# Performance work log

Measured on AMD Instinct MI355X. Metric: run time of the kernel, lower is better.

Reference implementation:

```python
import jax, jax.numpy as jnp
import numpy as np

B, S, H = 64, 512, 768
ATT_H, CLS_H = 100, 300


def setup_inputs() -> dict:
    key = jax.random.key(0)
    ks = jax.random.split(key, 8)
    hidden_states = jax.random.normal(ks[0], (B, S, H), jnp.float32)
    is_cont = jax.random.bernoulli(ks[1], 0.25, (B, S)).at[:, 0].set(False)
    offset_mapping = jnp.stack(
        [is_cont.astype(jnp.int32) * 3, jnp.zeros((B, S), jnp.int32)], axis=-1
    )
    labels = jax.random.randint(ks[2], (B, S), -1, 2).astype(jnp.float32)
    s = 0.02
    W1 = jax.random.normal(ks[3], (H, ATT_H), jnp.float32) * s
    b1 = jnp.zeros((ATT_H,), jnp.float32)
    W2 = jax.random.normal(ks[4], (ATT_H, 1), jnp.float32) * s
    b2 = jnp.zeros((1,), jnp.float32)
    W3 = jax.random.normal(ks[5], (H, CLS_H), jnp.float32) * s
    b3 = jnp.zeros((CLS_H,), jnp.float32)
    W4 = jax.random.normal(ks[6], (CLS_H, 1), jnp.float32) * s
    b4 = jnp.zeros((1,), jnp.float32)
    return dict(hidden_states=hidden_states, offset_mapping=offset_mapping,
                labels=labels, W1=W1, b1=b1, W2=W2, b2=b2, W3=W3, b3=b3,
                W4=W4, b4=b4)


def reference(hidden_states, offset_mapping, labels, W1, b1, W2, b2, W3, b3, W4, b4):
    beta = 1.0            # soft_attention_beta
    w_sent, w_tok, w_reg = 1.0, 1.0, 0.01
    Bn, Sn, _ = hidden_states.shape

    # token attention head: sigmoid(tanh(h W1 + b1) W2 + b2) -> [B, S]
    token_att = jax.nn.sigmoid(jnp.tanh(hidden_states @ W1 + b1) @ W2 + b2)[..., 0]

    # --- subword grouping as a single segment-max ---
    # a continuation token (offset[...,0] != 0) belongs to the segment started
    # by the previous non-continuation token (the word root).
    is_cont = offset_mapping[:, :, 0] != 0          # [B, S]
    start = jnp.logical_not(is_cont)
    start_flat = start.reshape(-1)
    seg_id = jnp.cumsum(start_flat.astype(jnp.int32)) - 1   # [B*S]
    vals = token_att.reshape(-1)
    seg_red = jax.ops.segment_max(vals, seg_id, num_segments=Bn * Sn)  # 'max' subword_method
    # scatter the group reduction back onto the word-root position only
    word_att = jnp.where(start_flat, seg_red[seg_id], vals).reshape(Bn, Sn)

    # mask: labelled (!= -1) AND not a subword continuation
    mask = (jnp.logical_and(labels != -1.0, start)).astype(hidden_states.dtype)
    masked = word_att * mask                          # token_logits

    # soft attention pooling over sequence
    p = jnp.power(masked, beta)
    norm = p / jnp.sum(p, axis=1, keepdims=True)      # [B, S]
    pooled = jnp.einsum('bsh,bs->bh', hidden_states, norm)

    sent = jax.nn.sigmoid(jnp.tanh(pooled @ W3 + b3) @ W4 + b4)  # [B, 1]

    # --- losses (_calculate_loss) ---
    sent_labels = jnp.max(labels, axis=1, keepdims=True)          # [B, 1]
    sentence_loss = jnp.sum((sent - sent_labels) ** 2)
    zero_labels = jnp.where(labels == 1.0, labels, 0.0)
    token_loss = jnp.sum((masked - zero_labels) ** 2)
    ones_mask = jnp.where(masked == 0.0, 1.0, masked)
    reg_a = jnp.sum(jnp.min(ones_mask, axis=1, keepdims=True) ** 2)
    reg_b = jnp.sum((jnp.max(masked, axis=1, keepdims=True) - sent_labels) ** 2)
    loss = w_sent * sentence_loss + w_tok * token_loss + w_reg * (reg_a + reg_b)

    return (loss, sentence_loss, token_loss, reg_a, reg_b,
            hidden_states, masked, sent)
```

## Files before the change

kernel.cpp:

```cpp
#include <hip/hip_runtime.h>
#include <math.h>

#define Bn 64
#define Sn 512
#define Hn 768
#define ATT_H 100
#define CLS_H 300
#define Mtok (Bn*Sn)
#define NP 112
#define NT 7

#define W1T_N (NP*Hn)
#define W3T_N (CLS_H*Hn)
#define POOL_N (Bn*Hn)

#define KCH 256
#define LDA2 264

typedef __attribute__((ext_vector_type(8))) short short8;
typedef __attribute__((ext_vector_type(4))) float floatx4;

__device__ inline float sigf(float x) { return 1.0f / (1.0f + expf(-x)); }

__device__ inline unsigned short f2bf(float x) {
    union { float f; unsigned int u; } v; v.f = x;
    unsigned int r = (v.u + 0x7FFFu + ((v.u >> 16) & 1u)) >> 16;
    return (unsigned short)r;
}

__device__ inline float wred_sum(float v) {
    #pragma unroll
    for (int d = 32; d; d >>= 1) v += __shfl_down(v, d, 64);
    return v;
}
__device__ inline float wred_max(float v) {
    #pragma unroll
    for (int d = 32; d; d >>= 1) v = fmaxf(v, __shfl_down(v, d, 64));
    return v;
}
__device__ inline float wred_min(float v) {
    #pragma unroll
    for (int d = 32; d; d >>= 1) v = fminf(v, __shfl_down(v, d, 64));
    return v;
}

__global__ __launch_bounds__(256) void k0_prep(
    const float* __restrict__ W1, const float* __restrict__ b1,
    const float* __restrict__ W2, const float* __restrict__ W3,
    unsigned short* __restrict__ w1t, float* __restrict__ b1w2,
    float* __restrict__ w3t, float* __restrict__ pooled,
    float* __restrict__ zpart)
{
    int idx = blockIdx.x * 256 + threadIdx.x;
    if (idx < W1T_N) {
        int n = idx / Hn, k = idx - n * Hn;
        float v = (n < ATT_H) ? W1[(size_t)k * ATT_H + n] : 0.f;
        w1t[idx] = f2bf(v);
    } else if (idx < W1T_N + W3T_N) {
        int i = idx - W1T_N;
        int j = i / Hn, k = i - j * Hn;
        w3t[i] = W3[(size_t)k * CLS_H + j];
    } else if (idx < W1T_N + W3T_N + NP) {
        int j = idx - (W1T_N + W3T_N);
        b1w2[2 * j]     = (j < ATT_H) ? b1[j] : 0.f;
        b1w2[2 * j + 1] = (j < ATT_H) ? W2[j] : 0.f;
    } else if (idx < W1T_N + W3T_N + NP + POOL_N) {
        pooled[idx - (W1T_N + W3T_N + NP)] = 0.f;
    } else if (idx < W1T_N + W3T_N + NP + POOL_N + 5 * Bn) {
        zpart[idx - (W1T_N + W3T_N + NP + POOL_N)] = 0.f;
    }
}

__global__ __launch_bounds__(512, 4) void k1_att(
    const float* __restrict__ h, const unsigned short* __restrict__ w1t,
    const float* __restrict__ b1w2, const float* __restrict__ b2,
    float* __restrict__ out_hidden, float* __restrict__ att)
{
    __shared__ unsigned short As[64 * LDA2];

    const int tid = threadIdx.x;
    const int wave = tid >> 6, lane = tid & 63;
    const int u = lane & 15, q = lane >> 4;
    const int tl = wave & 3, g = wave >> 2;
    const int t0 = blockIdx.x * 64;
    const int srow = tid >> 6, sc4 = tid & 63;

    floatx4 acc[NT];
    #pragma unroll
    for (int ct = 0; ct < NT; ct++) acc[ct] = (floatx4)0.f;

    for (int it = 0; it < 3; it++) {
        __syncthreads();
        #pragma unroll
        for (int j = 0; j < 8; j++) {
            int row = srow + j * 8;
            size_t gidx = (size_t)(t0 + row) * Hn + it * KCH + sc4 * 4;
            floatx4 v = *(const floatx4*)(h + gidx);
            *(floatx4*)(out_hidden + gidx) = v;
            ushort4 bv;
            bv.x = f2bf(v.x); bv.y = f2bf(v.y);
            bv.z = f2bf(v.z); bv.w = f2bf(v.w);
            *(ushort4*)(&As[row * LDA2 + sc4 * 4]) = bv;
        }
        __syncthreads();
        #pragma unroll
        for (int kk = 0; kk < 4; kk++) {
            short8 a = *(const short8*)(&As[(tl * 16 + u) * LDA2 + g * 128 + kk * 32 + q * 8]);
            #pragma unroll
            for (int ct = 0; ct < NT; ct++) {
                const short8* bp = (const short8*)(w1t + (size_t)(ct * 16 + u) * Hn
                                                   + it * KCH + g * 128 + kk * 32 + q * 8);
                acc[ct] = __builtin_amdgcn_mfma_f32_16x16x32_bf16(a, *bp, acc[ct], 0, 0, 0);
            }
        }
    }

    __syncthreads();
    float* cb = (float*)As;
    if (g == 1) {
        #pragma unroll
        for (int ct = 0; ct < NT; ct++)
            *(floatx4*)(&cb[(tl * 64 + lane) * 28 + ct * 4]) = acc[ct];
    }
    __syncthreads();
    if (g == 0) {
        #pragma unroll
        for (int ct = 0; ct < NT; ct++) {
            floatx4 o = *(const floatx4*)(&cb[(tl * 64 + lane) * 28 + ct * 4]);
            acc[ct] += o;
        }
        float z[4] = {0.f, 0.f, 0.f, 0.f};
        #pragma unroll
        for (int ct = 0; ct < NT; ct++) {
            float2 bw = *(const float2*)(b1w2 + (ct * 16 + u) * 2);
            #pragma unroll
            for (int r = 0; r < 4; r++)
                z[r] += tanhf(acc[ct][r] + bw.x) * bw.y;
        }
        #pragma unroll
        for (int mask = 1; mask < 16; mask <<= 1) {
            #pragma unroll
            for (int r = 0; r < 4; r++) z[r] += __shfl_xor(z[r], mask, 64);
        }
        if (u == 0) {
            float bb2 = b2[0];
            #pragma unroll
            for (int r = 0; r < 4; r++)
                att[t0 + tl * 16 + q * 4 + r] = sigf(z[r] + bb2);
        }
    }
}

__global__ __launch_bounds__(256) void k2_seg(
    const float* __restrict__ att, const int* __restrict__ offset,
    const float* __restrict__ labels, float* __restrict__ masked_out,
    float* __restrict__ sum_m, float* __restrict__ slab_o,
    float* __restrict__ tl_o, float* __restrict__ mino_o,
    float* __restrict__ maxm_o)
{
    const int b = blockIdx.x, tid = threadIdx.x;
    __shared__ float attl[Sn];
    __shared__ int   startl[Sn];
    __shared__ float v0[Sn], v1[Sn];
    __shared__ int   f0[Sn], f1[Sn];
    __shared__ float rsum[4], rtl[4], rsl[4], rmn[4], rmx[4];

    for (int s = tid; s < Sn; s += 256) {
        attl[s] = att[b * Sn + s];
        startl[s] = (offset[(size_t)(b * Sn + s) * 2] == 0) ? 1 : 0;
    }
    __syncthreads();
    for (int i = tid; i < Sn; i += 256) {
        int s = Sn - 1 - i;
        int endf = (s == Sn - 1) ? 1 : startl[s + 1];
        v0[i] = attl[s];
        f0[i] = endf;
    }
    __syncthreads();

    float* va = v0; float* vb = v1;
    int* fa = f0; int* fb = f1;
    for (int d = 1; d < Sn; d <<= 1) {
        for (int i = tid; i < Sn; i += 256) {
            float v = va[i]; int f = fa[i];
            float nv = v; int nf = f;
            if (i >= d) {
                if (!f) nv = fmaxf(v, va[i - d]);
                nf = f | fa[i - d];
            }
            vb[i] = nv; fb[i] = nf;
        }
        __syncthreads();
        float* tv = va; va = vb; vb = tv;
        int* tf = fa; fa = fb; fb = tf;
    }

    float lsum = 0.f, ltl = 0.f, lslab = -1e30f, lmin = 1e30f, lmax = -1e30f;
    for (int s = tid; s < Sn; s += 256) {
        float lab = labels[b * Sn + s];
        int st = startl[s];
        float segm = va[Sn - 1 - s];
        float m = (st && lab != -1.0f) ? segm : 0.f;
        masked_out[b * Sn + s] = m;
        lsum += m;
        float zl = (lab == 1.0f) ? 1.f : 0.f;
        ltl += (m - zl) * (m - zl);
        lslab = fmaxf(lslab, lab);
        float om = (m == 0.f) ? 1.f : m;
        lmin = fminf(lmin, om);
        lmax = fmaxf(lmax, m);
    }
    int wid = tid >> 6, lane = tid & 63;
    lsum = wred_sum(lsum); ltl = wred_sum(ltl);
    lslab = wred_max(lslab); lmin = wred_min(lmin); lmax = wred_max(lmax);
    if (lane == 0) { rsum[wid]=lsum; rtl[wid]=ltl; rsl[wid]=lslab; rmn[wid]=lmin; rmx[wid]=lmax; }
    __syncthreads();
    if (tid == 0) {
        sum_m[b]  = rsum[0]+rsum[1]+rsum[2]+rsum[3];
        tl_o[b]   = rtl[0]+rtl[1]+rtl[2]+rtl[3];
        slab_o[b] = fmaxf(fmaxf(rsl[0],rsl[1]), fmaxf(rsl[2],rsl[3]));
        mino_o[b] = fminf(fminf(rmn[0],rmn[1]), fminf(rmn[2],rmn[3]));
        maxm_o[b] = fmaxf(fmaxf(rmx[0],rmx[1]), fmaxf(rmx[2],rmx[3]));
    }
}

__global__ __launch_bounds__(192) void k3_pool(
    const float* __restrict__ h, const float* __restrict__ masked,
    const float* __restrict__ sum_m, float* __restrict__ pooled)
{
    const int b = blockIdx.x, sc = blockIdx.y;
    const int tid = threadIdx.x;
    __shared__ float nrm[16];
    if (tid < 16)
        nrm[tid] = masked[b * Sn + sc * 16 + tid] * (1.0f / sum_m[b]);
    __syncthreads();
    const floatx4* hp = (const floatx4*)(h + ((size_t)b * Sn + sc * 16) * Hn) + tid;
    float ax = 0.f, ay = 0.f, az = 0.f, aw = 0.f;
    #pragma unroll 8
    for (int s = 0; s < 16; s++) {
        floatx4 v = hp[(size_t)s * (Hn / 4)];
        float w = nrm[s];
        ax += v.x * w; ay += v.y * w; az += v.z * w; aw += v.w * w;
    }
    float* pp = pooled + (size_t)b * Hn + tid * 4;
    atomicAdd(pp + 0, ax); atomicAdd(pp + 1, ay);
    atomicAdd(pp + 2, az); atomicAdd(pp + 3, aw);
}

__global__ __launch_bounds__(256) void k4_sent(
    const float* __restrict__ pooled, const float* __restrict__ w3t,
    const float* __restrict__ b3, const float* __restrict__ W4,
    float* __restrict__ zpart)
{
    const int b = blockIdx.x, jc = blockIdx.y;
    const int tid = threadIdx.x;
    __shared__ __align__(16) float pl[Hn];
    __shared__ float yred[64];
    for (int k = tid; k < Hn; k += 256) pl[k] = pooled[(size_t)b * Hn + k];
    if (tid < 64) yred[tid] = 0.f;
    __syncthreads();
    int jj = tid >> 2, ks = tid & 3;
    float a = 0.f;
    if (jj < 60) {
        int j = jc * 60 + jj;
        const floatx4* wr = (const floatx4*)(w3t + (size_t)j * Hn) + ks * 48;
        const floatx4* pr = (const floatx4*)pl + ks * 48;
        #pragma unroll 8
        for (int i = 0; i < 48; i++) {
            floatx4 wv = wr[i]; floatx4 pv = pr[i];
            a += wv.x * pv.x + wv.y * pv.y + wv.z * pv.z + wv.w * pv.w;
        }
    }
    a += __shfl_xor(a, 1, 64);
    a += __shfl_xor(a, 2, 64);
    if (jj < 60 && ks == 0) {
        int j = jc * 60 + jj;
        yred[jj] = tanhf(a + b3[j]) * W4[j];
    }
    __syncthreads();
    if (tid < 64) {
        float y = yred[tid];
        y = wred_sum(y);
        if (tid == 0) zpart[jc * Bn + b] = y;
    }
}

__global__ __launch_bounds__(64) void k5_loss(
    const float* __restrict__ zpart, const float* __restrict__ b4,
    const float* __restrict__ slab, const float* __restrict__ tl,
    const float* __restrict__ mino, const float* __restrict__ maxm,
    float* __restrict__ out, float* __restrict__ out_sent)
{
    int t = threadIdx.x;
    float z = b4[0];
    #pragma unroll
    for (int jc = 0; jc < 5; jc++) z += zpart[jc * Bn + t];
    float sent = sigf(z);
    out_sent[t] = sent;
    float sl = slab[t];
    float e1 = (sent - sl) * (sent - sl);
    float e2 = tl[t];
    float e3 = mino[t] * mino[t];
    float mm = maxm[t] - sl;
    float e4 = mm * mm;
    e1 = wred_sum(e1); e2 = wred_sum(e2); e3 = wred_sum(e3); e4 = wred_sum(e4);
    if (t == 0) {
        out[1] = e1;
        out[2] = e2;
        out[3] = e3;
        out[4] = e4;
        out[0] = e1 + e2 + 0.01f * (e3 + e4);
    }
}

extern "C" void kernel_launch(void* const* d_in, const int* in_sizes, int n_in,
                              void* d_out, int out_size, void* d_ws, size_t ws_size,
                              hipStream_t stream) {
    (void)in_sizes; (void)n_in; (void)out_size; (void)ws_size;
    const float* h      = (const float*)d_in[0];
    const int*   offset = (const int*)d_in[1];
    const float* labels = (const float*)d_in[2];
    const float* W1     = (const float*)d_in[3];
    const float* b1     = (const float*)d_in[4];
    const float* W2     = (const float*)d_in[5];
    const float* b2     = (const float*)d_in[6];
    const float* W3     = (const float*)d_in[7];
    const float* b3     = (const float*)d_in[8];
    const float* W4     = (const float*)d_in[9];
    const float* b4     = (const float*)d_in[10];

    float* out        = (float*)d_out;
    float* out_hidden = out + 5;
    float* out_masked = out_hidden + (size_t)Bn * Sn * Hn;
    float* out_sent   = out_masked + (size_t)Bn * Sn;

    float* ws      = (float*)d_ws;
    float* att     = ws;
    float* sum_m   = att + Mtok;
    float* slab    = sum_m + Bn;
    float* tlb     = slab + Bn;
    float* mino    = tlb + Bn;
    float* maxm    = mino + Bn;
    float* pooled  = maxm + Bn;
    float* zpart   = pooled + POOL_N;
    float* b1w2    = zpart + 5 * Bn;
    float* w3t     = b1w2 + 2 * NP;
    unsigned short* w1t = (unsigned short*)(w3t + W3T_N);

    int k0_total = W1T_N + W3T_N + NP + POOL_N + 5 * Bn;
    k0_prep<<<(k0_total + 255) / 256, 256, 0, stream>>>(W1, b1, W2, W3,
                                                        w1t, b1w2, w3t, pooled, zpart);
    k1_att<<<Mtok / 64, 512, 0, stream>>>(h, w1t, b1w2, b2, out_hidden, att);
    k2_seg<<<Bn, 256, 0, stream>>>(att, offset, labels, out_masked,
                                   sum_m, slab, tlb, mino, maxm);
    k3_pool<<<dim3(Bn, 32), 192, 0, stream>>>(h, out_masked, sum_m, pooled);
    k4_sent<<<dim3(Bn, 5), 256, 0, stream>>>(pooled, w3t, b3, W4, zpart);
    k5_loss<<<1, 64, 0, stream>>>(zpart, b4, slab, tlb, mino, maxm, out, out_sent);
}
```

Measured before the change: 300.7 us.

## Load MFMA A-fragments directly from global and replace segment scan with serial walk

The attention kernel no longer stages bf16-converted hidden rows through shared memory. Each lane loads its 8 fp32 values straight from global, converts them in registers, copies them to the output and feeds the MFMA. Blocks shrink to 256 threads over 32 tokens, and the K split is two halves of 384. The segment-max kernel drops its log-step shared-memory scan and its barriers, and each word root instead walks forward over its continuation tokens serially. This trades fewer syncs and less LDS traffic for less coalesced global loads and a data-dependent serial loop.

Measured after the change: 335.5 us. +11.6%, slower.

```diff
diff --git a/kernel.cpp b/kernel.cpp
--- a/kernel.cpp
+++ b/kernel.cpp
@@ -13,9 +13,6 @@
 #define W1T_N (NP*Hn)
 #define W3T_N (CLS_H*Hn)
 #define POOL_N (Bn*Hn)
-
-#define KCH 256
-#define LDA2 264
 
 typedef __attribute__((ext_vector_type(8))) short short8;
 typedef __attribute__((ext_vector_type(4))) float floatx4;
@@ -71,52 +68,50 @@
     }
 }
 
-__global__ __launch_bounds__(512, 4) void k1_att(
+__global__ __launch_bounds__(256, 4) void k1_att(
     const float* __restrict__ h, const unsigned short* __restrict__ w1t,
     const float* __restrict__ b1w2, const float* __restrict__ b2,
     float* __restrict__ out_hidden, float* __restrict__ att)
 {
-    __shared__ unsigned short As[64 * LDA2];
+    __shared__ float cb[2 * 64 * 28];
 
     const int tid = threadIdx.x;
     const int wave = tid >> 6, lane = tid & 63;
     const int u = lane & 15, q = lane >> 4;
-    const int tl = wave & 3, g = wave >> 2;
-    const int t0 = blockIdx.x * 64;
-    const int srow = tid >> 6, sc4 = tid & 63;
+    const int tl = wave >> 1;
+    const int g  = wave & 1;
+    const int tok0 = blockIdx.x * 32 + tl * 16;
 
     floatx4 acc[NT];
     #pragma unroll
     for (int ct = 0; ct < NT; ct++) acc[ct] = (floatx4)0.f;
 
-    for (int it = 0; it < 3; it++) {
-        __syncthreads();
-        #pragma unroll
-        for (int j = 0; j < 8; j++) {
-            int row = srow + j * 8;
-            size_t gidx = (size_t)(t0 + row) * Hn + it * KCH + sc4 * 4;
-            floatx4 v = *(const floatx4*)(h + gidx);
-            *(floatx4*)(out_hidden + gidx) = v;
-            ushort4 bv;
-            bv.x = f2bf(v.x); bv.y = f2bf(v.y);
-            bv.z = f2bf(v.z); bv.w = f2bf(v.w);
-            *(ushort4*)(&As[row * LDA2 + sc4 * 4]) = bv;
-        }
-        __syncthreads();
-        #pragma unroll
-        for (int kk = 0; kk < 4; kk++) {
-            short8 a = *(const short8*)(&As[(tl * 16 + u) * LDA2 + g * 128 + kk * 32 + q * 8]);
-            #pragma unroll
-            for (int ct = 0; ct < NT; ct++) {
-                const short8* bp = (const short8*)(w1t + (size_t)(ct * 16 + u) * Hn
-                                                   + it * KCH + g * 128 + kk * 32 + q * 8);
-                acc[ct] = __builtin_amdgcn_mfma_f32_16x16x32_bf16(a, *bp, acc[ct], 0, 0, 0);
-            }
-        }
-    }
-
-    __syncthreads();
-    float* cb = (float*)As;
+    const size_t arow = (size_t)(tok0 + u) * Hn;
+    const int kbase = g * 384 + q * 8;
+
+    #pragma unroll 2
+    for (int ks = 0; ks < 12; ks++) {
+        const int k = kbase + ks * 32;
+        const float* ap = h + arow + k;
+        floatx4 v0 = *(const floatx4*)(ap);
+        floatx4 v1 = *(const floatx4*)(ap + 4);
+        *(floatx4*)(out_hidden + arow + k)     = v0;
+        *(floatx4*)(out_hidden + arow + k + 4) = v1;
+        short8 af;
+        af[0] = (short)f2bf(v0.x); af[1] = (short)f2bf(v0.y);
+        af[2] = (short)f2bf(v0.z); af[3] = (short)f2bf(v0.w);
+        af[4] = (short)f2bf(v1.x); af[5] = (short)f2bf(v1.y);
+        af[6] = (short)f2bf(v1.z); af[7] = (short)f2bf(v1.w);
+        short8 bf[NT];
+        #pragma unroll
+        for (int ct = 0; ct < NT; ct++)
+            bf[ct] = *(const short8*)(w1t + (size_t)(ct * 16 + u) * Hn + k);
+        #pragma unroll
+        for (int ct = 0; ct < NT; ct++)
+            acc[ct] = __builtin_amdgcn_mfma_f32_16x16x32_bf16(af, bf[ct], acc[ct], 0, 0, 0);
+    }
+
+    __syncthreads();
     if (g == 1) {
         #pragma unroll
         for (int ct = 0; ct < NT; ct++)
@@ -146,7 +141,7 @@
             float bb2 = b2[0];
             #pragma unroll
             for (int r = 0; r < 4; r++)
-                att[t0 + tl * 16 + q * 4 + r] = sigf(z[r] + bb2);
+                att[tok0 + q * 4 + r] = sigf(z[r] + bb2);
         }
     }
 }
@@ -161,8 +156,6 @@
     const int b = blockIdx.x, tid = threadIdx.x;
     __shared__ float attl[Sn];
     __shared__ int   startl[Sn];
-    __shared__ float v0[Sn], v1[Sn];
-    __shared__ int   f0[Sn], f1[Sn];
     __shared__ float rsum[4], rtl[4], rsl[4], rmn[4], rmx[4];
 
     for (int s = tid; s < Sn; s += 256) {
@@ -170,37 +163,17 @@
         startl[s] = (offset[(size_t)(b * Sn + s) * 2] == 0) ? 1 : 0;
     }
     __syncthreads();
-    for (int i = tid; i < Sn; i += 256) {
-        int s = Sn - 1 - i;
-        int endf = (s == Sn - 1) ? 1 : startl[s + 1];
-        v0[i] = attl[s];
-        f0[i] = endf;
-    }
-    __syncthreads();
-
-    float* va = v0; float* vb = v1;
-    int* fa = f0; int* fb = f1;
-    for (int d = 1; d < Sn; d <<= 1) {
-        for (int i = tid; i < Sn; i += 256) {
-            float v = va[i]; int f = fa[i];
-            float nv = v; int nf = f;
-            if (i >= d) {
-                if (!f) nv = fmaxf(v, va[i - d]);
-                nf = f | fa[i - d];
-            }
-            vb[i] = nv; fb[i] = nf;
-        }
-        __syncthreads();
-        float* tv = va; va = vb; vb = tv;
-        int* tf = fa; fa = fb; fb = tf;
-    }
 
     float lsum = 0.f, ltl = 0.f, lslab = -1e30f, lmin = 1e30f, lmax = -1e30f;
     for (int s = tid; s < Sn; s += 256) {
         float lab = labels[b * Sn + s];
         int st = startl[s];
-        float segm = va[Sn - 1 - s];
-        float m = (st && lab != -1.0f) ? segm : 0.f;
+        float m = 0.f;
+        if (st && lab != -1.0f) {
+            m = attl[s];
+            for (int t = s + 1; t < Sn && !startl[t]; t++)
+                m = fmaxf(m, attl[t]);
+        }
         masked_out[b * Sn + s] = m;
         lsum += m;
         float zl = (lab == 1.0f) ? 1.f : 0.f;
@@ -350,7 +323,7 @@
     int k0_total = W1T_N + W3T_N + NP + POOL_N + 5 * Bn;
     k0_prep<<<(k0_total + 255) / 256, 256, 0, stream>>>(W1, b1, W2, W3,
                                                         w1t, b1w2, w3t, pooled, zpart);
-    k1_att<<<Mtok / 64, 512, 0, stream>>>(h, w1t, b1w2, b2, out_hidden, att);
+    k1_att<<<Mtok / 32, 256, 0, stream>>>(h, w1t, b1w2, b2, out_hidden, att);
     k2_seg<<<Bn, 256, 0, stream>>>(att, offset, labels, out_masked,
                                    sum_m, slab, tlb, mino, maxm);
     k3_pool<<<dim3(Bn, 32), 192, 0, stream>>>(h, out_masked, sum_m, pooled);
```
